# Kernel tuning notes

Measured on AMD Instinct MI355X. Metric: run time of the kernel, lower is better.

The kernel has to match this reference:

```python
import jax, jax.numpy as jnp
import numpy as np

N_HEAD = 16

def setup_inputs() -> dict:
    key = jax.random.key(0)
    ks = jax.random.split(key, 5)
    C = 1024
    s = 0.02
    return {
        "x": jax.random.normal(ks[0], (4, 2048, C), dtype=jnp.float32),
        "w_attn": jax.random.normal(ks[1], (C, 3 * C), dtype=jnp.float32) * s,
        "b_attn": jnp.zeros((3 * C,), dtype=jnp.float32),
        "w_proj": jax.random.normal(ks[2], (C, C), dtype=jnp.float32) * s,
        "b_proj": jnp.zeros((C,), dtype=jnp.float32),
    }

def reference(x, w_attn, b_attn, w_proj, b_proj):
    B, T, C = x.shape
    H = N_HEAD
    D = C // H
    qkv = x @ w_attn + b_attn                      # [B,T,3C]
    q, k, v = jnp.split(qkv, 3, axis=-1)
    # [B,H,T,D]
    q = q.reshape(B, T, H, D).transpose(0, 2, 1, 3)
    k = k.reshape(B, T, H, D).transpose(0, 2, 1, 3)
    v = v.reshape(B, T, H, D).transpose(0, 2, 1, 3)
    scale = 1.0 / np.sqrt(D).astype(np.float32)
    attn = jnp.einsum('bhtd,bhsd->bhts', q, k) * scale   # [B,H,T,T]
    causal = jnp.tril(jnp.ones((T, T), dtype=bool))
    attn = jnp.where(causal, attn, -jnp.inf)
    attn = jax.nn.softmax(attn, axis=-1)
    y = jnp.einsum('bhts,bhsd->bhtd', attn, v)           # [B,H,T,D]
    y = y.transpose(0, 2, 1, 3).reshape(B, T, C)
    return y @ w_proj + b_proj
```

## Files before the change

kernel.cpp:

```cpp
#include <hip/hip_runtime.h>
#include <hip/hip_bf16.h>

typedef short short8 __attribute__((ext_vector_type(8)));
typedef float f32x4 __attribute__((ext_vector_type(4)));

typedef __attribute__((address_space(1))) void as1_void;
typedef __attribute__((address_space(3))) void as3_void;

__device__ __forceinline__ unsigned short f2bf(float f) {
    __hip_bfloat16 h = __float2bfloat16(f);
    return __builtin_bit_cast(unsigned short, h);
}

__device__ __forceinline__ float exp2fast(float x) {
    return __builtin_amdgcn_exp2f(x);
}

__device__ __forceinline__ void gload16(const unsigned short* g, unsigned short* l) {
    __builtin_amdgcn_global_load_lds((as1_void*)g, (as3_void*)l, 16, 0, 0);
}

__global__ __launch_bounds__(256) void conv_f32_to_bf16(
    const float* __restrict__ in, unsigned short* __restrict__ out, int n4) {
    int i = blockIdx.x * 256 + threadIdx.x;
    if (i >= n4) return;
    float4 v = ((const float4*)in)[i];
    ushort4 o;
    o.x = f2bf(v.x); o.y = f2bf(v.y); o.z = f2bf(v.z); o.w = f2bf(v.w);
    ((ushort4*)out)[i] = o;
}

__global__ __launch_bounds__(256) void transpose_f32_to_bf16(
    const float* __restrict__ W, unsigned short* __restrict__ WT, int K, int N) {
    __shared__ float tile[32][33];
    int tx = threadIdx.x, ty = threadIdx.y;
    int n0 = blockIdx.x * 32, k0 = blockIdx.y * 32;
#pragma unroll
    for (int j = 0; j < 4; ++j)
        tile[ty + j * 8][tx] = W[(size_t)(k0 + ty + j * 8) * N + n0 + tx];
    __syncthreads();
#pragma unroll
    for (int j = 0; j < 4; ++j)
        WT[(size_t)(n0 + ty + j * 8) * K + k0 + tx] = f2bf(tile[tx][ty + j * 8]);
}

template <int MODE>
__global__ __launch_bounds__(256, 2) void gemm_bt(
    const unsigned short* __restrict__ A,
    const unsigned short* __restrict__ Bt,
    const float* __restrict__ bias,
    void* __restrict__ out0,
    unsigned short* __restrict__ out1,
    int M, int N, int K) {
    __shared__ unsigned short sA[128 * 32];
    __shared__ unsigned short sB[128 * 32];
    const int tid = threadIdx.x;
    const int lane = tid & 63;
    const int w = tid >> 6;
    const int wr = (w >> 1) * 64;
    const int wc = (w & 1) * 64;
    const size_t arow0 = (size_t)blockIdx.x * 128;
    const size_t brow0 = (size_t)blockIdx.y * 128;

    const int grow = (w << 5) + (lane >> 2);
    const int gcol = (lane & 3) << 3;
    const unsigned short* pA0 = A + (arow0 + grow) * (size_t)K + gcol;
    const unsigned short* pB0 = Bt + (brow0 + grow) * (size_t)K + gcol;
    unsigned short* lA = sA + (w << 10);
    unsigned short* lB = sB + (w << 10);

    f32x4 acc[4][4] = {};
    const int fr = lane & 15;
    const int fk = (lane >> 4) << 3;

    for (int k0 = 0; k0 < K; k0 += 32) {
        __syncthreads();
        gload16(pA0 + k0, lA);
        gload16(pA0 + 16 * (size_t)K + k0, lA + 512);
        gload16(pB0 + k0, lB);
        gload16(pB0 + 16 * (size_t)K + k0, lB + 512);
        __syncthreads();

        short8 af[4], bfr[4];
#pragma unroll
        for (int i = 0; i < 4; ++i)
            af[i] = *(const short8*)&sA[(wr + i * 16 + fr) * 32 + fk];
#pragma unroll
        for (int i = 0; i < 4; ++i)
            bfr[i] = *(const short8*)&sB[(wc + i * 16 + fr) * 32 + fk];
#pragma unroll
        for (int mi = 0; mi < 4; ++mi)
#pragma unroll
            for (int ni = 0; ni < 4; ++ni)
                acc[mi][ni] = __builtin_amdgcn_mfma_f32_16x16x32_bf16(
                    af[mi], bfr[ni], acc[mi][ni], 0, 0, 0);
    }

    const int fq = (lane >> 4) << 2;
    if constexpr (MODE == 0) {
#pragma unroll
        for (int mi = 0; mi < 4; ++mi)
#pragma unroll
            for (int ni = 0; ni < 4; ++ni) {
                size_t r = arow0 + wr + mi * 16 + fq;
                size_t c = brow0 + wc + ni * 16 + fr;
                float bv = bias[c];
#pragma unroll
                for (int j = 0; j < 4; ++j)
                    ((float*)out0)[(r + j) * (size_t)N + c] = acc[mi][ni][j] + bv;
            }
    } else {
        const bool isv = (int)(brow0 + wc) >= 2048;
        if (isv) {
#pragma unroll
            for (int mi = 0; mi < 4; ++mi)
#pragma unroll
                for (int ni = 0; ni < 4; ++ni) {
                    int c = (int)brow0 + wc + ni * 16 + fr;
                    float bv = bias[c];
                    int cv = c - 2048;
                    int r0 = (int)arow0 + wr + mi * 16 + fq;
                    int bb = r0 >> 11, t0 = r0 & 2047;
                    unsigned int lo = (unsigned int)f2bf(acc[mi][ni][0] + bv) |
                                      ((unsigned int)f2bf(acc[mi][ni][1] + bv) << 16);
                    unsigned int hi = (unsigned int)f2bf(acc[mi][ni][2] + bv) |
                                      ((unsigned int)f2bf(acc[mi][ni][3] + bv) << 16);
                    *(uint2*)&out1[(((size_t)(bb * 1024 + cv)) << 11) + t0] =
                        make_uint2(lo, hi);
                }
        } else {
            const float qs = ((int)(brow0 + wc) < 1024) ? 0.125f * 1.4426950408889634f
                                                        : 1.0f;
#pragma unroll
            for (int mi = 0; mi < 4; ++mi)
#pragma unroll
                for (int ni = 0; ni < 4; ++ni) {
                    size_t r = arow0 + wr + mi * 16 + fq;
                    size_t c = brow0 + wc + ni * 16 + fr;
                    float bv = bias[c];
#pragma unroll
                    for (int j = 0; j < 4; ++j)
                        ((unsigned short*)out0)[(r + j) * 2048 + c] =
                            f2bf((acc[mi][ni][j] + bv) * qs);
                }
        }
    }
}

__global__ __launch_bounds__(256, 2) void attn_mfma(
    const unsigned short* __restrict__ qk,
    const unsigned short* __restrict__ vt,
    unsigned short* __restrict__ y,
    int BH) {
    constexpr int T = 2048;
    constexpr float THR = 8.0f;

    __shared__ __align__(16) unsigned short sK[2][64 * 64];
    __shared__ __align__(16) unsigned short sV[2][64 * 64];
    __shared__ __align__(16) unsigned short sP[4][32 * 64];

    const int tid = threadIdx.x;
    const int lane = tid & 63;
    const int w = tid >> 6;
    const int l15 = lane & 15;
    const int g = lane >> 4;

    const int bh = blockIdx.x % BH;
    const int qt = 15 - blockIdx.x / BH;
    const int b = bh >> 4;
    const int h = bh & 15;
    const int q0 = qt << 7;
    const int qw0 = q0 + w * 32;

    const unsigned short* kbase = qk + ((size_t)(b * T)) * 2048 + 1024 + h * 64;
    const unsigned short* vbase = vt + ((size_t)(b * 1024 + h * 64)) * 2048;
    unsigned short* sPw = sP[w];

    const int srow = tid >> 3;
    const int c16 = tid & 7;
    const int swz = ((c16 ^ (srow & 7)) << 3);

    short8 vones;
#pragma unroll
    for (int i = 0; i < 8; ++i) vones[i] = (short)0x3F80;

    short8 aq[2][2];
    {
        const unsigned short* qbase = qk + ((size_t)(b * T + qw0)) * 2048 + h * 64;
#pragma unroll
        for (int mi = 0; mi < 2; ++mi)
#pragma unroll
            for (int kc = 0; kc < 2; ++kc)
                aq[mi][kc] = *(const short8*)(qbase + (size_t)(mi * 16 + l15) * 2048 +
                                              g * 8 + kc * 32);
    }

    f32x4 O[2][4] = {};
    float m_st[2][4], l_st[2][4];
#pragma unroll
    for (int mi = 0; mi < 2; ++mi)
#pragma unroll
        for (int r = 0; r < 4; ++r) { m_st[mi][r] = -1e30f; l_st[mi][r] = 0.f; }

    const int nt = (q0 + 128) >> 6;

    uint4 kd0, kd1, vd0, vd1;
    kd0 = *(const uint4*)(kbase + (size_t)(srow) * 2048 + c16 * 8);
    kd1 = *(const uint4*)(kbase + (size_t)(srow + 32) * 2048 + c16 * 8);
    vd0 = *(const uint4*)(vbase + (size_t)srow * 2048 + c16 * 8);
    vd1 = *(const uint4*)(vbase + (size_t)(srow + 32) * 2048 + c16 * 8);
    *(uint4*)&sK[0][srow * 64 + swz] = kd0;
    *(uint4*)&sK[0][(srow + 32) * 64 + swz] = kd1;
    *(uint4*)&sV[0][srow * 64 + swz] = vd0;
    *(uint4*)&sV[0][(srow + 32) * 64 + swz] = vd1;
    __syncthreads();

    int cur = 0;
    for (int it = 0; it < nt; ++it) {
        const int s0 = it << 6;
        const bool haveNext = (it + 1 < nt);
        if (haveNext) {
            const int s1 = s0 + 64;
            kd0 = *(const uint4*)(kbase + (size_t)(s1 + srow) * 2048 + c16 * 8);
            kd1 = *(const uint4*)(kbase + (size_t)(s1 + srow + 32) * 2048 + c16 * 8);
            vd0 = *(const uint4*)(vbase + (size_t)srow * 2048 + s1 + c16 * 8);
            vd1 = *(const uint4*)(vbase + (size_t)(srow + 32) * 2048 + s1 + c16 * 8);
        }
        const unsigned short* sKc = sK[cur];
        const unsigned short* sVc = sV[cur];

        if (s0 <= qw0 + 31) {
            f32x4 sacc[2][4] = {};
            {
                short8 bk[4][2];
#pragma unroll
                for (int ni = 0; ni < 4; ++ni) {
                    const int row = ni * 16 + l15;
#pragma unroll
                    for (int kc = 0; kc < 2; ++kc)
                        bk[ni][kc] = *(const short8*)&sKc[row * 64 +
                                                          (((g + kc * 4) ^ (row & 7))
                                                           << 3)];
                }
                __builtin_amdgcn_s_setprio(1);
#pragma unroll
                for (int kc = 0; kc < 2; ++kc)
#pragma unroll
                    for (int mi = 0; mi < 2; ++mi)
#pragma unroll
                        for (int ni = 0; ni < 4; ++ni)
                            sacc[mi][ni] = __builtin_amdgcn_mfma_f32_16x16x32_bf16(
                                aq[mi][kc], bk[ni][kc], sacc[mi][ni], 0, 0, 0);
                __builtin_amdgcn_s_setprio(0);
            }

            const bool needMask = (s0 + 63 > qw0);
            float mxl[2][4];
            bool big = false;
#pragma unroll
            for (int mi = 0; mi < 2; ++mi) {
#pragma unroll
                for (int reg = 0; reg < 4; ++reg) {
                    if (needMask) {
                        const int qg = qw0 + mi * 16 + g * 4 + reg;
#pragma unroll
                        for (int ni = 0; ni < 4; ++ni) {
                            float v = sacc[mi][ni][reg];
                            sacc[mi][ni][reg] =
                                (s0 + ni * 16 + l15 <= qg) ? v : -INFINITY;
                        }
                    }
                    float mx = fmaxf(fmaxf(sacc[mi][0][reg], sacc[mi][1][reg]),
                                     fmaxf(sacc[mi][2][reg], sacc[mi][3][reg]));
                    mxl[mi][reg] = mx;
                    big = big || (mx > m_st[mi][reg] + THR);
                }
            }

            const bool resc = __any(big);
            float f_sc[2][4];
            if (resc) {
#pragma unroll
                for (int mi = 0; mi < 2; ++mi) {
#pragma unroll
                    for (int reg = 0; reg < 4; ++reg) {
                        float mx = mxl[mi][reg];
                        mx = fmaxf(mx, __shfl_xor(mx, 1));
                        mx = fmaxf(mx, __shfl_xor(mx, 2));
                        mx = fmaxf(mx, __shfl_xor(mx, 4));
                        mx = fmaxf(mx, __shfl_xor(mx, 8));
                        const float mn = fmaxf(m_st[mi][reg], mx);
                        f_sc[mi][reg] = exp2fast(m_st[mi][reg] - mn);
                        m_st[mi][reg] = mn;
                    }
                }
#pragma unroll
                for (int mi = 0; mi < 2; ++mi)
#pragma unroll
                    for (int di = 0; di < 4; ++di)
#pragma unroll
                        for (int reg = 0; reg < 4; ++reg)
                            O[mi][di][reg] *= f_sc[mi][reg];
            }

#pragma unroll
            for (int mi = 0; mi < 2; ++mi) {
#pragma unroll
                for (int reg = 0; reg < 4; ++reg) {
                    const int q_loc = mi * 16 + g * 4 + reg;
                    const float mrow = m_st[mi][reg];
#pragma unroll
                    for (int ni = 0; ni < 4; ++ni) {
                        float pv = exp2fast(sacc[mi][ni][reg] - mrow);
                        const int s = ni * 16 + l15;
                        sPw[q_loc * 64 + ((((s >> 3) ^ (q_loc & 7)) << 3) | (s & 7))] =
                            f2bf(pv);
                    }
                }
            }

            short8 aP[2][2], bv[4][2];
#pragma unroll
            for (int mi = 0; mi < 2; ++mi) {
                const int row = mi * 16 + l15;
#pragma unroll
                for (int kc = 0; kc < 2; ++kc)
                    aP[mi][kc] = *(const short8*)&sPw[row * 64 +
                                                      (((g + kc * 4) ^ (row & 7))
                                                       << 3)];
            }
#pragma unroll
            for (int di = 0; di < 4; ++di) {
                const int row = di * 16 + l15;
#pragma unroll
                for (int kc = 0; kc < 2; ++kc)
                    bv[di][kc] = *(const short8*)&sVc[row * 64 +
                                                      (((g + kc * 4) ^ (row & 7))
                                                       << 3)];
            }
            f32x4 lacc[2] = {};
            __builtin_amdgcn_s_setprio(1);
#pragma unroll
            for (int kc = 0; kc < 2; ++kc)
#pragma unroll
                for (int mi = 0; mi < 2; ++mi)
                    lacc[mi] = __builtin_amdgcn_mfma_f32_16x16x32_bf16(
                        aP[mi][kc], vones, lacc[mi], 0, 0, 0);
#pragma unroll
            for (int kc = 0; kc < 2; ++kc)
#pragma unroll
                for (int mi = 0; mi < 2; ++mi)
#pragma unroll
                    for (int di = 0; di < 4; ++di)
                        O[mi][di] = __builtin_amdgcn_mfma_f32_16x16x32_bf16(
                            aP[mi][kc], bv[di][kc], O[mi][di], 0, 0, 0);
            __builtin_amdgcn_s_setprio(0);
            if (resc) {
#pragma unroll
                for (int mi = 0; mi < 2; ++mi)
#pragma unroll
                    for (int reg = 0; reg < 4; ++reg)
                        l_st[mi][reg] =
                            l_st[mi][reg] * f_sc[mi][reg] + lacc[mi][reg];
            } else {
#pragma unroll
                for (int mi = 0; mi < 2; ++mi)
#pragma unroll
                    for (int reg = 0; reg < 4; ++reg)
                        l_st[mi][reg] += lacc[mi][reg];
            }
        }

        if (haveNext) {
            unsigned short* sKn = sK[cur ^ 1];
            unsigned short* sVn = sV[cur ^ 1];
            *(uint4*)&sKn[srow * 64 + swz] = kd0;
            *(uint4*)&sKn[(srow + 32) * 64 + swz] = kd1;
            *(uint4*)&sVn[srow * 64 + swz] = vd0;
            *(uint4*)&sVn[(srow + 32) * 64 + swz] = vd1;
        }
        __syncthreads();
        cur ^= 1;
    }

#pragma unroll
    for (int mi = 0; mi < 2; ++mi) {
#pragma unroll
        for (int reg = 0; reg < 4; ++reg) {
            const float inv = 1.0f / l_st[mi][reg];
            const int q = qw0 + mi * 16 + g * 4 + reg;
            const size_t base = (size_t)(b * T + q) * 1024 + h * 64 + l15;
#pragma unroll
            for (int di = 0; di < 4; ++di)
                y[base + di * 16] = f2bf(O[mi][di][reg] * inv);
        }
    }
}

extern "C" void kernel_launch(void* const* d_in, const int* in_sizes, int n_in,
                              void* d_out, int out_size, void* d_ws, size_t ws_size,
                              hipStream_t stream) {
    const float* x      = (const float*)d_in[0];
    const float* w_attn = (const float*)d_in[1];
    const float* b_attn = (const float*)d_in[2];
    const float* w_proj = (const float*)d_in[3];
    const float* b_proj = (const float*)d_in[4];

    const int C = 1024, T = 2048, H = 16;
    const int B = in_sizes[0] / (T * C);
    const int M = B * T;

    unsigned short* xb  = (unsigned short*)d_ws;
    unsigned short* wTa = xb + (size_t)M * C;
    unsigned short* wTp = wTa + (size_t)3 * C * C;
    unsigned short* qkb = wTp + (size_t)C * C;
    unsigned short* vtb = qkb + (size_t)M * 2 * C;
    unsigned short* y   = xb;

    int n4 = (M * C) / 4;
    conv_f32_to_bf16<<<(n4 + 255) / 256, 256, 0, stream>>>(x, xb, n4);
    transpose_f32_to_bf16<<<dim3(3 * C / 32, C / 32), dim3(32, 8), 0, stream>>>(
        w_attn, wTa, C, 3 * C);
    transpose_f32_to_bf16<<<dim3(C / 32, C / 32), dim3(32, 8), 0, stream>>>(
        w_proj, wTp, C, C);
    gemm_bt<2><<<dim3(M / 128, (3 * C) / 128), 256, 0, stream>>>(
        xb, wTa, b_attn, (void*)qkb, vtb, M, 3 * C, C);
    attn_mfma<<<dim3((B * H) * 16), 256, 0, stream>>>(qkb, vtb, y, B * H);
    gemm_bt<0><<<dim3(M / 128, C / 128), 256, 0, stream>>>(
        y, wTp, b_proj, d_out, nullptr, M, C, C);
}
```

Measured before the change: 187.3 us.

## Switch attention to 32x32x16 MFMA with transposed S and register-resident P

Rewrites the attention inner loop to use 32x32x16 bf16 MFMA and computes S transposed (K as A operand, Q as B), so each lane owns one query row and the row max needs a single cross-half shuffle. P is converted to bf16 with packed cvt and permlane32 swaps, so it stays in registers and the LDS round trip through the per-wave sP buffer is removed. Rescale factors are redistributed with ds_bpermute to match the O layout. This cuts LDS traffic and shuffle reductions, but depends on exact MFMA lane-layout assumptions and raises accumulator register pressure.

```diff
diff --git a/kernel.cpp b/kernel.cpp
--- a/kernel.cpp
+++ b/kernel.cpp
@@ -3,6 +3,7 @@
 
 typedef short short8 __attribute__((ext_vector_type(8)));
 typedef float f32x4 __attribute__((ext_vector_type(4)));
+typedef float f32x16 __attribute__((ext_vector_type(16)));
 
 typedef __attribute__((address_space(1))) void as1_void;
 typedef __attribute__((address_space(3))) void as3_void;
@@ -14,6 +15,16 @@
 
 __device__ __forceinline__ float exp2fast(float x) {
     return __builtin_amdgcn_exp2f(x);
+}
+
+__device__ __forceinline__ unsigned int cvtpk(float lo, float hi) {
+    unsigned int r;
+    asm("v_cvt_pk_bf16_f32 %0, %1, %2" : "=v"(r) : "v"(lo), "v"(hi));
+    return r;
+}
+
+__device__ __forceinline__ void plswap(unsigned int& a, unsigned int& b) {
+    asm("v_permlane32_swap_b32 %0, %1" : "+v"(a), "+v"(b));
 }
 
 __device__ __forceinline__ void gload16(const unsigned short* g, unsigned short* l) {
@@ -157,13 +168,12 @@
 
     __shared__ __align__(16) unsigned short sK[2][64 * 64];
     __shared__ __align__(16) unsigned short sV[2][64 * 64];
-    __shared__ __align__(16) unsigned short sP[4][32 * 64];
 
     const int tid = threadIdx.x;
     const int lane = tid & 63;
     const int w = tid >> 6;
-    const int l15 = lane & 15;
-    const int g = lane >> 4;
+    const int l31 = lane & 31;
+    const int b5 = lane >> 5;
 
     const int bh = blockIdx.x % BH;
     const int qt = 15 - blockIdx.x / BH;
@@ -174,7 +184,6 @@
 
     const unsigned short* kbase = qk + ((size_t)(b * T)) * 2048 + 1024 + h * 64;
     const unsigned short* vbase = vt + ((size_t)(b * 1024 + h * 64)) * 2048;
-    unsigned short* sPw = sP[w];
 
     const int srow = tid >> 3;
     const int c16 = tid & 7;
@@ -184,23 +193,18 @@
 #pragma unroll
     for (int i = 0; i < 8; ++i) vones[i] = (short)0x3F80;
 
-    short8 aq[2][2];
+    short8 aq[4];
     {
-        const unsigned short* qbase = qk + ((size_t)(b * T + qw0)) * 2048 + h * 64;
-#pragma unroll
-        for (int mi = 0; mi < 2; ++mi)
-#pragma unroll
-            for (int kc = 0; kc < 2; ++kc)
-                aq[mi][kc] = *(const short8*)(qbase + (size_t)(mi * 16 + l15) * 2048 +
-                                              g * 8 + kc * 32);
-    }
-
-    f32x4 O[2][4] = {};
-    float m_st[2][4], l_st[2][4];
-#pragma unroll
-    for (int mi = 0; mi < 2; ++mi)
-#pragma unroll
-        for (int r = 0; r < 4; ++r) { m_st[mi][r] = -1e30f; l_st[mi][r] = 0.f; }
+        const unsigned short* qbase =
+            qk + ((size_t)(b * T + qw0 + l31)) * 2048 + h * 64;
+#pragma unroll
+        for (int kc = 0; kc < 4; ++kc)
+            aq[kc] = *(const short8*)(qbase + b5 * 8 + kc * 16);
+    }
+
+    f32x16 O0 = {}, O1 = {};
+    f32x16 l_st = {};
+    float m_st = -1e30f;
 
     const int nt = (q0 + 128) >> 6;
 
@@ -230,145 +234,111 @@
         const unsigned short* sVc = sV[cur];
 
         if (s0 <= qw0 + 31) {
-            f32x4 sacc[2][4] = {};
-            {
-                short8 bk[4][2];
-#pragma unroll
-                for (int ni = 0; ni < 4; ++ni) {
-                    const int row = ni * 16 + l15;
-#pragma unroll
-                    for (int kc = 0; kc < 2; ++kc)
-                        bk[ni][kc] = *(const short8*)&sKc[row * 64 +
-                                                          (((g + kc * 4) ^ (row & 7))
-                                                           << 3)];
-                }
-                __builtin_amdgcn_s_setprio(1);
-#pragma unroll
-                for (int kc = 0; kc < 2; ++kc)
-#pragma unroll
-                    for (int mi = 0; mi < 2; ++mi)
-#pragma unroll
-                        for (int ni = 0; ni < 4; ++ni)
-                            sacc[mi][ni] = __builtin_amdgcn_mfma_f32_16x16x32_bf16(
-                                aq[mi][kc], bk[ni][kc], sacc[mi][ni], 0, 0, 0);
-                __builtin_amdgcn_s_setprio(0);
-            }
+            f32x16 sacc[2] = {};
+            __builtin_amdgcn_s_setprio(1);
+#pragma unroll
+            for (int kc = 0; kc < 4; ++kc) {
+#pragma unroll
+                for (int ni = 0; ni < 2; ++ni) {
+                    const int row = ni * 32 + l31;
+                    short8 akf = *(const short8*)&sKc[row * 64 +
+                                                      (((b5 + kc * 2) ^ (row & 7))
+                                                       << 3)];
+                    sacc[ni] = __builtin_amdgcn_mfma_f32_32x32x16_bf16(
+                        akf, aq[kc], sacc[ni], 0, 0, 0);
+                }
+            }
+            __builtin_amdgcn_s_setprio(0);
 
             const bool needMask = (s0 + 63 > qw0);
-            float mxl[2][4];
-            bool big = false;
-#pragma unroll
-            for (int mi = 0; mi < 2; ++mi) {
-#pragma unroll
-                for (int reg = 0; reg < 4; ++reg) {
-                    if (needMask) {
-                        const int qg = qw0 + mi * 16 + g * 4 + reg;
-#pragma unroll
-                        for (int ni = 0; ni < 4; ++ni) {
-                            float v = sacc[mi][ni][reg];
-                            sacc[mi][ni][reg] =
-                                (s0 + ni * 16 + l15 <= qg) ? v : -INFINITY;
-                        }
+            const int qg = qw0 + l31;
+            if (needMask) {
+#pragma unroll
+                for (int ni = 0; ni < 2; ++ni)
+#pragma unroll
+                    for (int reg = 0; reg < 16; ++reg) {
+                        const int sg = s0 + ni * 32 + (reg & 3) + 8 * (reg >> 2) +
+                                       4 * b5;
+                        sacc[ni][reg] = (sg <= qg) ? sacc[ni][reg] : -INFINITY;
                     }
-                    float mx = fmaxf(fmaxf(sacc[mi][0][reg], sacc[mi][1][reg]),
-                                     fmaxf(sacc[mi][2][reg], sacc[mi][3][reg]));
-                    mxl[mi][reg] = mx;
-                    big = big || (mx > m_st[mi][reg] + THR);
-                }
-            }
-
-            const bool resc = __any(big);
-            float f_sc[2][4];
+            }
+
+            float mx = sacc[0][0];
+#pragma unroll
+            for (int reg = 1; reg < 16; ++reg) mx = fmaxf(mx, sacc[0][reg]);
+#pragma unroll
+            for (int reg = 0; reg < 16; ++reg) mx = fmaxf(mx, sacc[1][reg]);
+            mx = fmaxf(mx, __shfl_xor(mx, 32));
+
+            const bool resc = __any(mx > m_st + THR);
+            float f_l = 1.0f;
             if (resc) {
-#pragma unroll
-                for (int mi = 0; mi < 2; ++mi) {
-#pragma unroll
-                    for (int reg = 0; reg < 4; ++reg) {
-                        float mx = mxl[mi][reg];
-                        mx = fmaxf(mx, __shfl_xor(mx, 1));
-                        mx = fmaxf(mx, __shfl_xor(mx, 2));
-                        mx = fmaxf(mx, __shfl_xor(mx, 4));
-                        mx = fmaxf(mx, __shfl_xor(mx, 8));
-                        const float mn = fmaxf(m_st[mi][reg], mx);
-                        f_sc[mi][reg] = exp2fast(m_st[mi][reg] - mn);
-                        m_st[mi][reg] = mn;
-                    }
-                }
-#pragma unroll
-                for (int mi = 0; mi < 2; ++mi)
-#pragma unroll
-                    for (int di = 0; di < 4; ++di)
-#pragma unroll
-                        for (int reg = 0; reg < 4; ++reg)
-                            O[mi][di][reg] *= f_sc[mi][reg];
-            }
-
-#pragma unroll
-            for (int mi = 0; mi < 2; ++mi) {
-#pragma unroll
-                for (int reg = 0; reg < 4; ++reg) {
-                    const int q_loc = mi * 16 + g * 4 + reg;
-                    const float mrow = m_st[mi][reg];
-#pragma unroll
-                    for (int ni = 0; ni < 4; ++ni) {
-                        float pv = exp2fast(sacc[mi][ni][reg] - mrow);
-                        const int s = ni * 16 + l15;
-                        sPw[q_loc * 64 + ((((s >> 3) ^ (q_loc & 7)) << 3) | (s & 7))] =
-                            f2bf(pv);
-                    }
-                }
-            }
-
-            short8 aP[2][2], bv[4][2];
-#pragma unroll
-            for (int mi = 0; mi < 2; ++mi) {
-                const int row = mi * 16 + l15;
-#pragma unroll
-                for (int kc = 0; kc < 2; ++kc)
-                    aP[mi][kc] = *(const short8*)&sPw[row * 64 +
-                                                      (((g + kc * 4) ^ (row & 7))
+                const float mn = fmaxf(m_st, mx);
+                f_l = exp2fast(m_st - mn);
+                m_st = mn;
+            }
+
+#pragma unroll
+            for (int ni = 0; ni < 2; ++ni)
+#pragma unroll
+                for (int reg = 0; reg < 16; ++reg)
+                    sacc[ni][reg] = exp2fast(sacc[ni][reg] - m_st);
+
+            short8 pa[4];
+#pragma unroll
+            for (int c = 0; c < 4; ++c) {
+                const int ni = c >> 1;
+                const int off = (c & 1) * 8;
+                unsigned int pk01 = cvtpk(sacc[ni][off + 0], sacc[ni][off + 1]);
+                unsigned int pk23 = cvtpk(sacc[ni][off + 2], sacc[ni][off + 3]);
+                unsigned int pk45 = cvtpk(sacc[ni][off + 4], sacc[ni][off + 5]);
+                unsigned int pk67 = cvtpk(sacc[ni][off + 6], sacc[ni][off + 7]);
+                plswap(pk01, pk45);
+                plswap(pk23, pk67);
+                uint4 u = make_uint4(pk01, pk23, pk45, pk67);
+                pa[c] = __builtin_bit_cast(short8, u);
+            }
+
+            if (resc) {
+                const int fil = __builtin_bit_cast(int, f_l);
+#pragma unroll
+                for (int reg = 0; reg < 16; ++reg) {
+                    const int qpat = (reg & 3) + 8 * (reg >> 2) + 4 * b5;
+                    const float fq = __builtin_bit_cast(
+                        float, __builtin_amdgcn_ds_bpermute(
+                                   (qpat + (lane & 32)) << 2, fil));
+                    O0[reg] *= fq;
+                    O1[reg] *= fq;
+                    l_st[reg] *= fq;
+                }
+            }
+
+            f32x16 lacc = {};
+            __builtin_amdgcn_s_setprio(1);
+#pragma unroll
+            for (int c = 0; c < 4; ++c) {
+                lacc = __builtin_amdgcn_mfma_f32_32x32x16_bf16(
+                    pa[c], vones, lacc, 0, 0, 0);
+                {
+                    const int row = l31;
+                    short8 bvf = *(const short8*)&sVc[row * 64 +
+                                                      (((c * 2 + b5) ^ (row & 7))
                                                        << 3)];
-            }
-#pragma unroll
-            for (int di = 0; di < 4; ++di) {
-                const int row = di * 16 + l15;
-#pragma unroll
-                for (int kc = 0; kc < 2; ++kc)
-                    bv[di][kc] = *(const short8*)&sVc[row * 64 +
-                                                      (((g + kc * 4) ^ (row & 7))
+                    O0 = __builtin_amdgcn_mfma_f32_32x32x16_bf16(
+                        pa[c], bvf, O0, 0, 0, 0);
+                }
+                {
+                    const int row = 32 + l31;
+                    short8 bvf = *(const short8*)&sVc[row * 64 +
+                                                      (((c * 2 + b5) ^ (row & 7))
                                                        << 3)];
-            }
-            f32x4 lacc[2] = {};
-            __builtin_amdgcn_s_setprio(1);
-#pragma unroll
-            for (int kc = 0; kc < 2; ++kc)
-#pragma unroll
-                for (int mi = 0; mi < 2; ++mi)
-                    lacc[mi] = __builtin_amdgcn_mfma_f32_16x16x32_bf16(
-                        aP[mi][kc], vones, lacc[mi], 0, 0, 0);
-#pragma unroll
-            for (int kc = 0; kc < 2; ++kc)
-#pragma unroll
-                for (int mi = 0; mi < 2; ++mi)
-#pragma unroll
-                    for (int di = 0; di < 4; ++di)
-                        O[mi][di] = __builtin_amdgcn_mfma_f32_16x16x32_bf16(
-                            aP[mi][kc], bv[di][kc], O[mi][di], 0, 0, 0);
+                    O1 = __builtin_amdgcn_mfma_f32_32x32x16_bf16(
+                        pa[c], bvf, O1, 0, 0, 0);
+                }
+            }
             __builtin_amdgcn_s_setprio(0);
-            if (resc) {
-#pragma unroll
-                for (int mi = 0; mi < 2; ++mi)
-#pragma unroll
-                    for (int reg = 0; reg < 4; ++reg)
-                        l_st[mi][reg] =
-                            l_st[mi][reg] * f_sc[mi][reg] + lacc[mi][reg];
-            } else {
-#pragma unroll
-                for (int mi = 0; mi < 2; ++mi)
-#pragma unroll
-                    for (int reg = 0; reg < 4; ++reg)
-                        l_st[mi][reg] += lacc[mi][reg];
-            }
+#pragma unroll
+            for (int reg = 0; reg < 16; ++reg) l_st[reg] += lacc[reg];
         }
 
         if (haveNext) {
@@ -384,16 +354,12 @@
     }
 
 #pragma unroll
-    for (int mi = 0; mi < 2; ++mi) {
-#pragma unroll
-        for (int reg = 0; reg < 4; ++reg) {
-            const float inv = 1.0f / l_st[mi][reg];
-            const int q = qw0 + mi * 16 + g * 4 + reg;
-            const size_t base = (size_t)(b * T + q) * 1024 + h * 64 + l15;
-#pragma unroll
-            for (int di = 0; di < 4; ++di)
-                y[base + di * 16] = f2bf(O[mi][di][reg] * inv);
-        }
+    for (int reg = 0; reg < 16; ++reg) {
+        const int qpat = (reg & 3) + 8 * (reg >> 2) + 4 * b5;
+        const float inv = 1.0f / l_st[reg];
+        const size_t base = (size_t)(b * T + qw0 + qpat) * 1024 + h * 64 + l31;
+        y[base] = f2bf(O0[reg] * inv);
+        y[base + 32] = f2bf(O1[reg] * inv);
     }
 }
 
```

Result: faster. 173.4 us (-7.4%).
